# Kernel optimization log

Measured on AMD Instinct MI355X. Metric: run time of the kernel, lower is better.

## Reference

```python
import jax, jax.numpy as jnp
import numpy as np

SCORE_THRESH = 0.05
NMS_THRESH = 0.5
MAX_DET = 100
N_BOXES = 8192


def setup_inputs() -> dict:
    key = jax.random.key(0)
    k1, k2, k3, k4, k5 = jax.random.split(key, 5)
    N = N_BOXES
    # well-formed axis-aligned boxes (x1,y1,x2,y2) plus 8 keypoint coords
    xy = jax.random.uniform(k1, (N, 2)) * 1000.0
    wh = jax.random.uniform(k2, (N, 2)) * 120.0 + 4.0
    kp = jax.random.uniform(k3, (N, 8)) * 1000.0
    boxes = jnp.concatenate([xy, xy + wh, kp], axis=1)            # (N, 12)
    classification = jax.random.uniform(k4, (N, 8))               # two heads x 4 orientations
    dimensions = jax.random.uniform(k5, (N, 3)) * 4.0             # (h, w, l) for the single class
    return {"boxes": boxes, "dimensions": dimensions, "classification": classification}


def _nms_keep(b4, scores, valid):
    """Greedy NMS. Returns (order, keep) where order sorts by score desc and
    keep[i] says whether the i-th sorted box survives."""
    N = b4.shape[0]
    order = jnp.argsort(-jnp.where(valid, scores, -jnp.inf))
    bs = b4[order]                                                 # (N, 4) sorted boxes
    vs = valid[order]
    x1, y1, x2, y2 = bs[:, 0], bs[:, 1], bs[:, 2], bs[:, 3]
    area = (x2 - x1) * (y2 - y1)
    iw = jnp.clip(jnp.minimum(x2[:, None], x2[None, :]) - jnp.maximum(x1[:, None], x1[None, :]), 0.0)
    ih = jnp.clip(jnp.minimum(y2[:, None], y2[None, :]) - jnp.maximum(y1[:, None], y1[None, :]), 0.0)
    inter = iw * ih                                                # (N, N)
    iou = inter / jnp.maximum(area[:, None] + area[None, :] - inter, 1e-8)
    idx = jnp.arange(N)

    def body(keep, xs):
        row, v, i = xs
        suppressed = jnp.any(keep & (row > NMS_THRESH) & (idx < i))
        keep = keep.at[i].set(v & jnp.logical_not(suppressed))
        return keep, None

    keep, _ = jax.lax.scan(body, jnp.zeros((N,), dtype=bool), (iou, vs, idx))
    return order, keep


def reference(boxes, dimensions, classification):
    # max over the two classification heads -> per-orientation score (N, 4)
    cls2 = jnp.maximum(classification[:, :4], classification[:, 4:])
    orient = jnp.argmax(cls2, axis=1)                              # best orientation per box
    score = jnp.max(cls2, axis=1)                                  # best-orientation score
    valid = score > SCORE_THRESH

    order, keep = _nms_keep(boxes[:, :4], score, valid)
    sorted_score = jnp.where(keep, score[order], -jnp.inf)
    top_scores, top_pos = jax.lax.top_k(sorted_score, MAX_DET)     # top-k among kept
    sel = order[top_pos]                                           # original box indices
    ok = jnp.isfinite(top_scores)                                  # real detections vs -1 padding

    out_boxes = jnp.where(ok[:, None], boxes[sel], -1.0)           # (MAX_DET, 12)
    out_dims = jnp.where(ok[:, None], dimensions[sel, :3], -1.0)   # (MAX_DET, 3)
    out_scores = jnp.where(ok, score[sel], -1.0)                   # (MAX_DET,)
    out_labels = jnp.where(ok, 0, -1).astype(jnp.int32)            # single class -> label 0
    out_orient = jnp.where(ok, orient[sel], -1).astype(jnp.int32)
    return out_boxes, out_dims, out_scores, out_labels, out_orient
```

## Files before the change

kernel.cpp:

```cpp
#include <hip/hip_runtime.h>

#define NBOX 8192
#define BT 1024
#define MAXDET 100
#define SCORE_T 0.05f
#define NMS_T 0.5f
#define CAP 1024
#define CAPM 384
#define NWMAX 6
#define KTGT 128
#define TOPBIN_T 0.99609375f

typedef unsigned long long u64;

__device__ __forceinline__ float rl_f(float v, int j) {
    return __int_as_float(__builtin_amdgcn_readlane(__float_as_int(v), j));
}

__device__ __forceinline__ float iou_fn(float x1, float y1, float x2, float y2, float area,
                                        float bx1, float by1, float bx2, float by2, float barea) {
    float iw = fminf(x2, bx2) - fmaxf(x1, bx1);
    float ih = fminf(y2, by2) - fmaxf(y1, by1);
    iw = fmaxf(iw, 0.0f);
    ih = fmaxf(ih, 0.0f);
    float inter = iw * ih;
    return inter / fmaxf(area + barea - inter, 1e-8f);
}

__device__ __forceinline__ void bins_of(unsigned k, int& b1, int& b2) {
    float s = __uint_as_float(k & 0x7FFFFFFFu);
    b1 = (int)(s * 256.0f); if (b1 > 255) b1 = 255;
    b2 = (int)(s * 65536.0f) & 255;
}

__global__ __launch_bounds__(BT) void hot_kernel(
    const float* __restrict__ boxes, const float* __restrict__ dims,
    const float* __restrict__ cls, unsigned* __restrict__ flagG,
    float* __restrict__ out) {
    __shared__ u64 s_sel[CAPM];
    __shared__ float4 s_cb[CAPM];
    __shared__ unsigned char s_or[CAPM];
    __shared__ u64 s_gt[NWMAX][CAPM];
    __shared__ u64 s_sg[NWMAX][CAPM];
    __shared__ u64 s_K[NWMAX], s_U[NWMAX];
    __shared__ int s_cnt;

    const int tid = threadIdx.x;
    const int lane = tid & 63;
    const int w = tid >> 6;

    if (tid == 0) s_cnt = 0;
    __syncthreads();

#pragma unroll
    for (int j = 0; j < NBOX / BT; ++j) {
        int i = tid + j * BT;
        const float4 c0 = *reinterpret_cast<const float4*>(cls + i * 8);
        const float4 c1 = *reinterpret_cast<const float4*>(cls + i * 8 + 4);
        float m0 = fmaxf(c0.x, c1.x), m1 = fmaxf(c0.y, c1.y);
        float m2 = fmaxf(c0.z, c1.z), m3 = fmaxf(c0.w, c1.w);
        float s = fmaxf(fmaxf(m0, m1), fmaxf(m2, m3));
        if (s > SCORE_T && s >= TOPBIN_T) {
            unsigned u = __float_as_uint(s);
            unsigned key = (u >> 31) ? ~u : (u | 0x80000000u);
            int o = 0; float best = m0;
            if (m1 > best) { best = m1; o = 1; }
            if (m2 > best) { best = m2; o = 2; }
            if (m3 > best) { best = m3; o = 3; }
            int pos = atomicAdd(&s_cnt, 1);
            if (pos < CAPM) {
                s_sel[pos] = (((u64)key) << 13) | (unsigned)(NBOX - 1 - i);
                s_cb[pos] = *reinterpret_cast<const float4*>(boxes + i * 12);
                s_or[pos] = (unsigned char)o;
            }
        }
    }
    __syncthreads();
    const int cnt = s_cnt;
    if (cnt == 0 || cnt > CAPM) {
        if (tid == 0) flagG[0] = 1u;
        return;
    }
    const int NW = (cnt + 63) >> 6;

    const int tot = NW * cnt;
    for (int p = tid; p < tot; p += BT) {
        int q = p / cnt;
        int t = p - q * cnt;
        u64 selt = s_sel[t];
        float4 bt = s_cb[t];
        float x1 = bt.x, y1 = bt.y, x2 = bt.z, y2 = bt.w;
        float area = (x2 - x1) * (y2 - y1);
        int jbase = q << 6;
        int jmax = cnt - jbase; if (jmax > 64) jmax = 64;
        u64 g = 0ull, sg = 0ull;
        for (int jj = 0; jj < jmax; ++jj) {
            int jdx = jbase + jj;
            u64 selj = s_sel[jdx];
            float4 bj = s_cb[jdx];
            float barea = (bj.z - bj.x) * (bj.w - bj.y);
            float iou = iou_fn(x1, y1, x2, y2, area, bj.x, bj.y, bj.z, bj.w, barea);
            if (selj > selt) {
                u64 bit = 1ull << jj;
                g |= bit;
                if (iou > NMS_T) sg |= bit;
            }
        }
        s_gt[q][t] = g;
        s_sg[q][t] = sg;
    }
    if (tid < NWMAX) {
        int base = tid << 6;
        u64 uw = (cnt <= base) ? 0ull
               : ((cnt - base >= 64) ? ~0ull : ((1ull << (cnt - base)) - 1ull));
        s_U[tid] = uw;
        s_K[tid] = 0ull;
    }
    __syncthreads();

    const int t = tid;
    const bool have = t < cnt;
    for (int it = 0; it < CAPM; ++it) {
        bool undec = have && ((s_U[t >> 6] >> (t & 63)) & 1ull);
        u64 deadm = 0ull, blkm = 0ull;
        if (undec) {
            for (int q = 0; q < NW; ++q) {
                u64 sg = s_sg[q][t];
                deadm |= sg & s_K[q];
                blkm  |= sg & s_U[q];
            }
        }
        bool toDead = undec && (deadm != 0ull);
        bool toKept = undec && (deadm == 0ull) && (blkm == 0ull);
        u64 dW = __ballot(toDead);
        u64 kW = __ballot(toKept);
        if (lane == 0 && w < NW) {
            s_K[w] |= kW;
            s_U[w] &= ~(kW | dW);
        }
        __syncthreads();
        u64 anyU = 0ull;
        for (int q = 0; q < NW; ++q) anyU |= s_U[q];
        if (anyU == 0ull) break;
        __syncthreads();
    }

    int kcnt = 0;
    for (int q = 0; q < NW; ++q) kcnt += (int)__popcll(s_K[q]);
    if (kcnt < MAXDET) {
        if (tid == 0) flagG[0] = 1u;
        return;
    }
    if (tid == 0) flagG[0] = 0u;

    float* ob = out;
    float* od = out + MAXDET * 12;
    float* os = out + MAXDET * 15;
    float* ol = out + MAXDET * 16;
    float* oo = out + MAXDET * 17;
    if (have && ((s_K[t >> 6] >> (t & 63)) & 1ull)) {
        int rank = 0;
        for (int q = 0; q < NW; ++q) rank += (int)__popcll(s_gt[q][t] & s_K[q]);
        if (rank < MAXDET) {
            u64 v = s_sel[t];
            int idx = NBOX - 1 - (int)(v & 8191ull);
            float sscore = __uint_as_float(((unsigned)(v >> 13)) & 0x7FFFFFFFu);
            float4* obr = reinterpret_cast<float4*>(ob + rank * 12);
            const float4* br = reinterpret_cast<const float4*>(boxes + idx * 12);
            obr[0] = s_cb[t];
            obr[1] = br[1];
            obr[2] = br[2];
            od[rank * 3 + 0] = dims[idx * 3 + 0];
            od[rank * 3 + 1] = dims[idx * 3 + 1];
            od[rank * 3 + 2] = dims[idx * 3 + 2];
            os[rank] = sscore;
            ol[rank] = 0.0f;
            oo[rank] = (float)s_or[t];
        }
    }
}

__global__ __launch_bounds__(BT) void fallback_kernel(
    const float* __restrict__ boxes, const float* __restrict__ dims,
    const float* __restrict__ cls, const unsigned* __restrict__ flagG,
    float* __restrict__ out) {
    if (flagG[0] == 0u) return;
    __shared__ unsigned s_key[NBOX];
    __shared__ unsigned s_hist[256];
    __shared__ u64 s_sel[CAP];
    __shared__ u64 s_srt[CAP];
    __shared__ unsigned short s_srtpos[CAP];
    __shared__ float4 s_cb[CAP];
    __shared__ float4 s_bb[128];
    __shared__ float s_bar[128];
    __shared__ float4 s_kb[MAXDET];
    __shared__ float s_karea[MAXDET], s_kscore[MAXDET];
    __shared__ int s_ksel[MAXDET];
    __shared__ int s_kc, s_cnt, s_B1, s_B2, s_state, s_refKrem;
    __shared__ u64 s_alive0;

    const int tid = threadIdx.x;
    const int lane = tid & 63;
    const int wid = tid >> 6;

    auto rank_scatter = [&](int sc, bool loadBox) {
        if (tid < sc) {
            u64 mine = s_sel[tid];
            float4 pb = make_float4(0.f, 0.f, 0.f, 0.f);
            if (loadBox) {
                int bidx = NBOX - 1 - (int)(mine & 8191ull);
                pb = *reinterpret_cast<const float4*>(boxes + bidx * 12);
            }
            int rank = 0;
            int j = 0;
            for (; j + 8 <= sc; j += 8) {
                u64 a0 = s_sel[j + 0], a1 = s_sel[j + 1], a2 = s_sel[j + 2], a3 = s_sel[j + 3];
                u64 a4 = s_sel[j + 4], a5 = s_sel[j + 5], a6 = s_sel[j + 6], a7 = s_sel[j + 7];
                rank += (int)(a0 > mine) + (int)(a1 > mine) + (int)(a2 > mine) + (int)(a3 > mine)
                      + (int)(a4 > mine) + (int)(a5 > mine) + (int)(a6 > mine) + (int)(a7 > mine);
            }
            for (; j < sc; ++j) rank += (s_sel[j] > mine) ? 1 : 0;
            s_srt[rank] = mine;
            s_srtpos[rank] = (unsigned short)tid;
            if (loadBox) s_cb[tid] = pb;
        }
    };

    auto nms_groups = [&](int scN) {
        for (int base = 0; base < scN && s_kc < MAXDET; base += 128) {
            const int kc0 = s_kc;
            float x1 = 0.f, y1 = 0.f, x2 = 0.f, y2 = 0.f, area = 0.f, sscore = 0.f;
            int sidx = 0; bool have = false;
            if (wid < 2) {
                int p = base + wid * 64 + lane;
                have = p < scN;
                u64 v = have ? s_srt[p] : 0ull;
                int cp = have ? (int)s_srtpos[p] : 0;
                sidx = NBOX - 1 - (int)(v & 8191ull);
                sscore = __uint_as_float(((unsigned)(v >> 13)) & 0x7FFFFFFFu);
                float4 b = s_cb[cp];
                if (have) { x1 = b.x; y1 = b.y; x2 = b.z; y2 = b.w; area = (x2 - x1) * (y2 - y1); }
                int sl = wid * 64 + lane;
                s_bb[sl] = make_float4(x1, y1, x2, y2); s_bar[sl] = area;
            }
            __syncthreads();
            if (wid == 0) {
                bool cand = have;
                for (int k = 0; k < kc0; ++k) {
                    float4 kb = s_kb[k];
                    float iou = iou_fn(x1, y1, x2, y2, area, kb.x, kb.y, kb.z, kb.w, s_karea[k]);
                    cand = cand && !(iou > NMS_T);
                }
                u64 m = 0ull;
#pragma unroll 8
                for (int j = 0; j < 64; ++j) {
                    float iou = iou_fn(x1, y1, x2, y2, area,
                                       rl_f(x1, j), rl_f(y1, j), rl_f(x2, j), rl_f(y2, j), rl_f(area, j));
                    if ((iou > NMS_T) && (j < lane)) m |= (1ull << j);
                }
                u64 alive = __ballot(cand);
                u64 conf = __ballot((m & alive) != 0ull) & alive;
                while (conf) {
                    int i = (int)__builtin_ctzll(conf);
                    bool deadI = (lane == i) && ((m & alive) != 0ull);
                    u64 d = __ballot(deadI);
                    alive &= ~d; conf &= ~(d | (1ull << i));
                }
                int rank = (int)__popcll(alive & ((1ull << lane) - 1ull));
                int slot = kc0 + rank;
                if (((alive >> lane) & 1ull) && slot < MAXDET) {
                    s_kb[slot] = make_float4(x1, y1, x2, y2);
                    s_karea[slot] = area; s_kscore[slot] = sscore; s_ksel[slot] = sidx;
                }
                if (lane == 0) s_alive0 = alive;
            }
            u64 m_low = 0ull, m_high = 0ull;
            bool cand1 = have;
            if (wid == 1) {
                for (int k = 0; k < kc0; ++k) {
                    float4 kb = s_kb[k];
                    float iou = iou_fn(x1, y1, x2, y2, area, kb.x, kb.y, kb.z, kb.w, s_karea[k]);
                    cand1 = cand1 && !(iou > NMS_T);
                }
#pragma unroll 8
                for (int j = 0; j < 64; ++j) {
                    float4 bb = s_bb[j];
                    float iou = iou_fn(x1, y1, x2, y2, area, bb.x, bb.y, bb.z, bb.w, s_bar[j]);
                    if (iou > NMS_T) m_low |= (1ull << j);
                }
#pragma unroll 8
                for (int j = 0; j < 64; ++j) {
                    float iou = iou_fn(x1, y1, x2, y2, area,
                                       rl_f(x1, j), rl_f(y1, j), rl_f(x2, j), rl_f(y2, j), rl_f(area, j));
                    if ((iou > NMS_T) && (j < lane)) m_high |= (1ull << j);
                }
            }
            __syncthreads();
            if (wid == 1) {
                u64 alive0 = s_alive0;
                int popc0 = (int)__popcll(alive0);
                bool cand = cand1 && ((m_low & alive0) == 0ull);
                u64 alive = __ballot(cand);
                u64 conf = __ballot((m_high & alive) != 0ull) & alive;
                while (conf) {
                    int i = (int)__builtin_ctzll(conf);
                    bool deadI = (lane == i) && ((m_high & alive) != 0ull);
                    u64 d = __ballot(deadI);
                    alive &= ~d; conf &= ~(d | (1ull << i));
                }
                int rank = (int)__popcll(alive & ((1ull << lane) - 1ull));
                int slot = kc0 + popc0 + rank;
                if (((alive >> lane) & 1ull) && slot < MAXDET) {
                    s_kb[slot] = make_float4(x1, y1, x2, y2);
                    s_karea[slot] = area; s_kscore[slot] = sscore; s_ksel[slot] = sidx;
                }
                if (lane == 0) {
                    int nk = kc0 + popc0 + (int)__popcll(alive);
                    s_kc = nk > MAXDET ? MAXDET : nk;
                }
            }
            __syncthreads();
        }
    };

    unsigned keyr[8];
#pragma unroll
    for (int j = 0; j < NBOX / BT; ++j) {
        int i = tid + j * BT;
        const float4 c0 = *reinterpret_cast<const float4*>(cls + i * 8);
        const float4 c1 = *reinterpret_cast<const float4*>(cls + i * 8 + 4);
        float s = fmaxf(fmaxf(fmaxf(c0.x, c1.x), fmaxf(c0.y, c1.y)),
                        fmaxf(fmaxf(c0.z, c1.z), fmaxf(c0.w, c1.w)));
        unsigned u = __float_as_uint(s);
        unsigned key = (u >> 31) ? ~u : (u | 0x80000000u);
        key = (s > SCORE_T) ? key : 0u;
        keyr[j] = key;
        s_key[i] = key;
    }
    if (tid == 0) { s_kc = 0; s_cnt = 0; }
    __syncthreads();
#pragma unroll
    for (int j = 0; j < NBOX / BT; ++j) {
        unsigned k = keyr[j];
        if (k) {
            float s = __uint_as_float(k & 0x7FFFFFFFu);
            if (s >= TOPBIN_T) {
                int pos = atomicAdd(&s_cnt, 1);
                if (pos < CAP) {
                    int i = tid + j * BT;
                    s_sel[pos] = (((u64)k) << 13) | (unsigned)(NBOX - 1 - i);
                    s_cb[pos] = *reinterpret_cast<const float4*>(boxes + i * 12);
                }
            }
        }
    }
    __syncthreads();
    const int cnt0 = s_cnt;
    const bool ovf = cnt0 > CAP;
    if (!ovf && cnt0 > 0) {
        rank_scatter(cnt0, false);
        __syncthreads();
        nms_groups(cnt0);
    }
    int U1 = ovf ? 256 : 255;
    int U2 = 0;
    if (s_kc < MAXDET) {
        if (tid < 256) s_hist[tid] = 0u;
        if (tid == 0) s_cnt = 0;
        __syncthreads();
        for (int j = 0; j < NBOX / BT; ++j) {
            unsigned k = s_key[tid + j * BT];
            if (k) {
                int b1, b2; bins_of(k, b1, b2);
                if (b1 < U1 || (b1 == U1 && b2 < U2)) atomicAdd(&s_hist[b1], 1u);
            }
        }
        while (true) {
            __syncthreads();
            if (wid == 0) {
                unsigned c0 = s_hist[lane * 4 + 0], c1s = s_hist[lane * 4 + 1];
                unsigned c2 = s_hist[lane * 4 + 2], c3 = s_hist[lane * 4 + 3];
                unsigned t3 = c3, t2 = c2 + t3, t1 = c1s + t2, t0 = c0 + t1;
                unsigned acc = t0;
#pragma unroll
                for (int d = 1; d < 64; d <<= 1) {
                    unsigned o = __shfl_down(acc, d);
                    if (lane + d < 64) acc += o;
                }
                unsigned excl = acc - t0;
                unsigned totalRem = __shfl(acc, 0);
                if (lane == 0) s_state = (totalRem == 0u) ? 2 : 0;
                if (totalRem != 0u) {
                    unsigned Kt = totalRem < (unsigned)KTGT ? totalRem : (unsigned)KTGT;
                    unsigned incq[4] = { excl + t0, excl + t1, excl + t2, excl + t3 };
                    unsigned abvq[4] = { excl + t1, excl + t2, excl + t3, excl };
#pragma unroll
                    for (int q = 0; q < 4; ++q) {
                        if (incq[q] >= Kt && abvq[q] < Kt) {
                            s_B1 = lane * 4 + q; s_B2 = 0;
                            if (incq[q] > CAP) { s_state = 1; s_refKrem = (int)(Kt - abvq[q]); }
                        }
                    }
                }
            }
            __syncthreads();
            const int st = s_state;
            if (st == 2) break;
            const int B1 = s_B1;
            if (st == 1) {
                if (tid < 256) s_hist[tid] = 0u;
                __syncthreads();
                for (int j = 0; j < NBOX / BT; ++j) {
                    unsigned k = s_key[tid + j * BT];
                    if (k) {
                        int b1, b2; bins_of(k, b1, b2);
                        if ((b1 < U1 || (b1 == U1 && b2 < U2)) && b1 == B1)
                            atomicAdd(&s_hist[b2], 1u);
                    }
                }
                __syncthreads();
                if (wid == 0) {
                    unsigned c0 = s_hist[lane * 4 + 0], c1s = s_hist[lane * 4 + 1];
                    unsigned c2 = s_hist[lane * 4 + 2], c3 = s_hist[lane * 4 + 3];
                    unsigned t3 = c3, t2 = c2 + t3, t1 = c1s + t2, t0 = c0 + t1;
                    unsigned acc = t0;
#pragma unroll
                    for (int d = 1; d < 64; d <<= 1) {
                        unsigned o = __shfl_down(acc, d);
                        if (lane + d < 64) acc += o;
                    }
                    unsigned excl = acc - t0;
                    unsigned Krem = (unsigned)s_refKrem;
                    unsigned incq[4] = { excl + t0, excl + t1, excl + t2, excl + t3 };
                    unsigned abvq[4] = { excl + t1, excl + t2, excl + t3, excl };
#pragma unroll
                    for (int q = 0; q < 4; ++q)
                        if (incq[q] >= Krem && abvq[q] < Krem) s_B2 = lane * 4 + q;
                }
                __syncthreads();
            }
            const int B2 = s_B2;
            for (int j = 0; j < NBOX / BT; ++j) {
                int i = tid + j * BT;
                unsigned k = s_key[i];
                if (k) {
                    int b1, b2; bins_of(k, b1, b2);
                    bool inr = (b1 < U1) || (b1 == U1 && b2 < U2);
                    bool sel = inr && ((b1 > B1) || (b1 == B1 && b2 >= B2));
                    if (sel) {
                        int pos = atomicAdd(&s_cnt, 1);
                        if (pos < CAP)
                            s_sel[pos] = (((u64)k) << 13) | (unsigned)(NBOX - 1 - i);
                    }
                }
            }
            __syncthreads();
            const int sc2 = s_cnt < CAP ? s_cnt : CAP;
            rank_scatter(sc2, true);
            __syncthreads();
            nms_groups(sc2);
            if (s_kc >= MAXDET) break;
            U1 = B1; U2 = B2;
            if (tid < 256) s_hist[tid] = 0u;
            if (tid == 0) s_cnt = 0;
            __syncthreads();
            for (int j = 0; j < NBOX / BT; ++j) {
                unsigned k = s_key[tid + j * BT];
                if (k) {
                    int b1, b2; bins_of(k, b1, b2);
                    if (b1 < U1 || (b1 == U1 && b2 < U2)) atomicAdd(&s_hist[b1], 1u);
                }
            }
        }
    }
    __syncthreads();
    if (tid < MAXDET) {
        const int kc = s_kc;
        float* ob = out;
        float* od = out + MAXDET * 12;
        float* os = out + MAXDET * 15;
        float* ol = out + MAXDET * 16;
        float* oo = out + MAXDET * 17;
        float4* obr = reinterpret_cast<float4*>(ob + tid * 12);
        if (tid < kc) {
            int sel = s_ksel[tid];
            const float4* br = reinterpret_cast<const float4*>(boxes + sel * 12);
            obr[0] = br[0]; obr[1] = br[1]; obr[2] = br[2];
            od[tid * 3 + 0] = dims[sel * 3 + 0];
            od[tid * 3 + 1] = dims[sel * 3 + 1];
            od[tid * 3 + 2] = dims[sel * 3 + 2];
            os[tid] = s_kscore[tid];
            ol[tid] = 0.0f;
            const float4 c0 = *reinterpret_cast<const float4*>(cls + sel * 8);
            const float4 c1 = *reinterpret_cast<const float4*>(cls + sel * 8 + 4);
            float m0 = fmaxf(c0.x, c1.x), m1 = fmaxf(c0.y, c1.y);
            float m2 = fmaxf(c0.z, c1.z), m3 = fmaxf(c0.w, c1.w);
            int o = 0; float best = m0;
            if (m1 > best) { best = m1; o = 1; }
            if (m2 > best) { best = m2; o = 2; }
            if (m3 > best) { best = m3; o = 3; }
            oo[tid] = (float)o;
        } else {
            const float4 neg1 = make_float4(-1.f, -1.f, -1.f, -1.f);
            obr[0] = neg1; obr[1] = neg1; obr[2] = neg1;
            od[tid * 3 + 0] = -1.0f; od[tid * 3 + 1] = -1.0f; od[tid * 3 + 2] = -1.0f;
            os[tid] = -1.0f; ol[tid] = -1.0f; oo[tid] = -1.0f;
        }
    }
}

extern "C" void kernel_launch(void* const* d_in, const int* in_sizes, int n_in,
                              void* d_out, int out_size, void* d_ws, size_t ws_size,
                              hipStream_t stream) {
    const float* boxes = (const float*)d_in[0];
    const float* dims  = (const float*)d_in[1];
    const float* cls   = (const float*)d_in[2];
    float* out = (float*)d_out;
    unsigned* flag = (unsigned*)d_ws;
    (void)in_sizes; (void)n_in; (void)out_size; (void)ws_size;
    hot_kernel<<<1, BT, 0, stream>>>(boxes, dims, cls, flag, out);
    fallback_kernel<<<1, BT, 0, stream>>>(boxes, dims, cls, flag, out);
}
```

Before: 27.74 us.

## Fuse hot and fallback NMS into one multi-block kernel with last-block finish

Replaces the single-block hot kernel and the separate fallback launch with one kernel over 32 blocks of 384 threads. Each block scores a 256-box slice and appends top-bin candidates to a global list via atomics. The last block to finish, detected with a done counter, runs the bitmask NMS or the histogram fallback. This spreads the initial score scan across CUs and removes one kernel launch, at the cost of a memset, global atomics and threadfences, and a smaller final block for the serial NMS phase.

```diff
diff --git a/kernel.cpp b/kernel.cpp
--- a/kernel.cpp
+++ b/kernel.cpp
@@ -1,7 +1,8 @@
 #include <hip/hip_runtime.h>
 
 #define NBOX 8192
-#define BT 1024
+#define NBLK 32
+#define BTF 384
 #define MAXDET 100
 #define SCORE_T 0.05f
 #define NMS_T 0.5f
@@ -33,28 +34,40 @@
     b2 = (int)(s * 65536.0f) & 255;
 }
 
-__global__ __launch_bounds__(BT) void hot_kernel(
+__global__ __launch_bounds__(BTF) void fused_kernel(
     const float* __restrict__ boxes, const float* __restrict__ dims,
-    const float* __restrict__ cls, unsigned* __restrict__ flagG,
+    const float* __restrict__ cls, unsigned* __restrict__ cntG,
+    unsigned* __restrict__ doneG, u64* __restrict__ kidxG,
     float* __restrict__ out) {
-    __shared__ u64 s_sel[CAPM];
-    __shared__ float4 s_cb[CAPM];
-    __shared__ unsigned char s_or[CAPM];
+    __shared__ u64 s_sel[CAP];
+    __shared__ float4 s_cb[CAP];
     __shared__ u64 s_gt[NWMAX][CAPM];
     __shared__ u64 s_sg[NWMAX][CAPM];
     __shared__ u64 s_K[NWMAX], s_U[NWMAX];
-    __shared__ int s_cnt;
+    __shared__ unsigned s_keyS[NBOX];
+    __shared__ unsigned s_hist[256];
+    __shared__ u64 s_srt[CAP];
+    __shared__ unsigned short s_srtpos[CAP];
+    __shared__ float4 s_bb[128];
+    __shared__ float s_bar[128];
+    __shared__ float4 s_kb[MAXDET];
+    __shared__ float s_karea[MAXDET], s_kscore[MAXDET];
+    __shared__ int s_ksel[MAXDET];
+    __shared__ int s_kc, s_cnt, s_B1, s_B2, s_state, s_refKrem;
+    __shared__ u64 s_alive0;
+    __shared__ int s_lcnt, s_base, s_last;
 
     const int tid = threadIdx.x;
     const int lane = tid & 63;
     const int w = tid >> 6;
-
-    if (tid == 0) s_cnt = 0;
+    const int blk = blockIdx.x;
+
+    if (tid == 0) s_lcnt = 0;
     __syncthreads();
-
-#pragma unroll
-    for (int j = 0; j < NBOX / BT; ++j) {
-        int i = tid + j * BT;
+    u64 myv = 0ull;
+    int lpos = -1;
+    if (tid < 256) {
+        const int i = blk * 256 + tid;
         const float4 c0 = *reinterpret_cast<const float4*>(cls + i * 8);
         const float4 c1 = *reinterpret_cast<const float4*>(cls + i * 8 + 4);
         float m0 = fmaxf(c0.x, c1.x), m1 = fmaxf(c0.y, c1.y);
@@ -63,321 +76,274 @@
         if (s > SCORE_T && s >= TOPBIN_T) {
             unsigned u = __float_as_uint(s);
             unsigned key = (u >> 31) ? ~u : (u | 0x80000000u);
-            int o = 0; float best = m0;
-            if (m1 > best) { best = m1; o = 1; }
-            if (m2 > best) { best = m2; o = 2; }
-            if (m3 > best) { best = m3; o = 3; }
-            int pos = atomicAdd(&s_cnt, 1);
-            if (pos < CAPM) {
-                s_sel[pos] = (((u64)key) << 13) | (unsigned)(NBOX - 1 - i);
-                s_cb[pos] = *reinterpret_cast<const float4*>(boxes + i * 12);
-                s_or[pos] = (unsigned char)o;
-            }
+            myv = (((u64)key) << 13) | (unsigned)(NBOX - 1 - i);
+            lpos = atomicAdd(&s_lcnt, 1);
         }
     }
     __syncthreads();
-    const int cnt = s_cnt;
-    if (cnt == 0 || cnt > CAPM) {
-        if (tid == 0) flagG[0] = 1u;
-        return;
+    if (tid == 0) s_base = (int)atomicAdd(cntG, (unsigned)s_lcnt);
+    __syncthreads();
+    if (lpos >= 0) {
+        int g = s_base + lpos;
+        if (g < CAPM) atomicExch(&kidxG[g], myv);
     }
-    const int NW = (cnt + 63) >> 6;
-
-    const int tot = NW * cnt;
-    for (int p = tid; p < tot; p += BT) {
-        int q = p / cnt;
-        int t = p - q * cnt;
-        u64 selt = s_sel[t];
-        float4 bt = s_cb[t];
-        float x1 = bt.x, y1 = bt.y, x2 = bt.z, y2 = bt.w;
-        float area = (x2 - x1) * (y2 - y1);
-        int jbase = q << 6;
-        int jmax = cnt - jbase; if (jmax > 64) jmax = 64;
-        u64 g = 0ull, sg = 0ull;
-        for (int jj = 0; jj < jmax; ++jj) {
-            int jdx = jbase + jj;
-            u64 selj = s_sel[jdx];
-            float4 bj = s_cb[jdx];
-            float barea = (bj.z - bj.x) * (bj.w - bj.y);
-            float iou = iou_fn(x1, y1, x2, y2, area, bj.x, bj.y, bj.z, bj.w, barea);
-            if (selj > selt) {
-                u64 bit = 1ull << jj;
-                g |= bit;
-                if (iou > NMS_T) sg |= bit;
-            }
-        }
-        s_gt[q][t] = g;
-        s_sg[q][t] = sg;
+    __threadfence();
+    __syncthreads();
+    if (tid == 0) s_last = (atomicAdd(doneG, 1u) == (unsigned)(NBLK - 1)) ? 1 : 0;
+    __syncthreads();
+    if (!s_last) return;
+    __threadfence();
+
+    const int cnt = (int)atomicAdd(cntG, 0u);
+
+    if (cnt > 0 && cnt <= CAPM) {
+        for (int t = tid; t < cnt; t += BTF) {
+            u64 v = atomicAdd(&kidxG[t], 0ull);
+            s_sel[t] = v;
+            int idx = NBOX - 1 - (int)(v & 8191ull);
+            s_cb[t] = *reinterpret_cast<const float4*>(boxes + idx * 12);
+        }
+        __syncthreads();
+        const int NW = (cnt + 63) >> 6;
+        const int tot = NW * cnt;
+        for (int p = tid; p < tot; p += BTF) {
+            int q = p / cnt;
+            int t = p - q * cnt;
+            u64 selt = s_sel[t];
+            float4 bt = s_cb[t];
+            float x1 = bt.x, y1 = bt.y, x2 = bt.z, y2 = bt.w;
+            float area = (x2 - x1) * (y2 - y1);
+            int jbase = q << 6;
+            int jmax = cnt - jbase; if (jmax > 64) jmax = 64;
+            u64 g = 0ull, sg = 0ull;
+            for (int jj = 0; jj < jmax; ++jj) {
+                int jdx = jbase + jj;
+                u64 selj = s_sel[jdx];
+                float4 bj = s_cb[jdx];
+                float barea = (bj.z - bj.x) * (bj.w - bj.y);
+                float iou = iou_fn(x1, y1, x2, y2, area, bj.x, bj.y, bj.z, bj.w, barea);
+                if (selj > selt) {
+                    u64 bit = 1ull << jj;
+                    g |= bit;
+                    if (iou > NMS_T) sg |= bit;
+                }
+            }
+            s_gt[q][t] = g;
+            s_sg[q][t] = sg;
+        }
+        if (tid < NWMAX) {
+            int base = tid << 6;
+            u64 uw = (cnt <= base) ? 0ull
+                   : ((cnt - base >= 64) ? ~0ull : ((1ull << (cnt - base)) - 1ull));
+            s_U[tid] = uw;
+            s_K[tid] = 0ull;
+        }
+        __syncthreads();
+        const int t = tid;
+        const bool have = t < cnt;
+        for (int it = 0; it < CAPM; ++it) {
+            bool undec = have && ((s_U[t >> 6] >> (t & 63)) & 1ull);
+            u64 deadm = 0ull, blkm = 0ull;
+            if (undec) {
+                for (int q = 0; q < NW; ++q) {
+                    u64 sg = s_sg[q][t];
+                    deadm |= sg & s_K[q];
+                    blkm  |= sg & s_U[q];
+                }
+            }
+            bool toDead = undec && (deadm != 0ull);
+            bool toKept = undec && (deadm == 0ull) && (blkm == 0ull);
+            u64 dW = __ballot(toDead);
+            u64 kW = __ballot(toKept);
+            if (lane == 0 && w < NW) {
+                s_K[w] |= kW;
+                s_U[w] &= ~(kW | dW);
+            }
+            __syncthreads();
+            u64 anyU = 0ull;
+            for (int q = 0; q < NW; ++q) anyU |= s_U[q];
+            if (anyU == 0ull) break;
+            __syncthreads();
+        }
+        int kcnt = 0;
+        for (int q = 0; q < NW; ++q) kcnt += (int)__popcll(s_K[q]);
+        if (kcnt >= MAXDET) {
+            float* ob = out;
+            float* od = out + MAXDET * 12;
+            float* os = out + MAXDET * 15;
+            float* ol = out + MAXDET * 16;
+            float* oo = out + MAXDET * 17;
+            if (have && ((s_K[t >> 6] >> (t & 63)) & 1ull)) {
+                int rank = 0;
+                for (int q = 0; q < NW; ++q) rank += (int)__popcll(s_gt[q][t] & s_K[q]);
+                if (rank < MAXDET) {
+                    u64 v = s_sel[t];
+                    int idx = NBOX - 1 - (int)(v & 8191ull);
+                    float sscore = __uint_as_float(((unsigned)(v >> 13)) & 0x7FFFFFFFu);
+                    float4* obr = reinterpret_cast<float4*>(ob + rank * 12);
+                    const float4* br = reinterpret_cast<const float4*>(boxes + idx * 12);
+                    obr[0] = s_cb[t];
+                    obr[1] = br[1];
+                    obr[2] = br[2];
+                    od[rank * 3 + 0] = dims[idx * 3 + 0];
+                    od[rank * 3 + 1] = dims[idx * 3 + 1];
+                    od[rank * 3 + 2] = dims[idx * 3 + 2];
+                    os[rank] = sscore;
+                    ol[rank] = 0.0f;
+                    const float4 c0 = *reinterpret_cast<const float4*>(cls + idx * 8);
+                    const float4 c1 = *reinterpret_cast<const float4*>(cls + idx * 8 + 4);
+                    float m0 = fmaxf(c0.x, c1.x), m1 = fmaxf(c0.y, c1.y);
+                    float m2 = fmaxf(c0.z, c1.z), m3 = fmaxf(c0.w, c1.w);
+                    int o = 0; float best = m0;
+                    if (m1 > best) { best = m1; o = 1; }
+                    if (m2 > best) { best = m2; o = 2; }
+                    if (m3 > best) { best = m3; o = 3; }
+                    oo[rank] = (float)o;
+                }
+            }
+            return;
+        }
     }
-    if (tid < NWMAX) {
-        int base = tid << 6;
-        u64 uw = (cnt <= base) ? 0ull
-               : ((cnt - base >= 64) ? ~0ull : ((1ull << (cnt - base)) - 1ull));
-        s_U[tid] = uw;
-        s_K[tid] = 0ull;
-    }
-    __syncthreads();
-
-    const int t = tid;
-    const bool have = t < cnt;
-    for (int it = 0; it < CAPM; ++it) {
-        bool undec = have && ((s_U[t >> 6] >> (t & 63)) & 1ull);
-        u64 deadm = 0ull, blkm = 0ull;
-        if (undec) {
-            for (int q = 0; q < NW; ++q) {
-                u64 sg = s_sg[q][t];
-                deadm |= sg & s_K[q];
-                blkm  |= sg & s_U[q];
-            }
-        }
-        bool toDead = undec && (deadm != 0ull);
-        bool toKept = undec && (deadm == 0ull) && (blkm == 0ull);
-        u64 dW = __ballot(toDead);
-        u64 kW = __ballot(toKept);
-        if (lane == 0 && w < NW) {
-            s_K[w] |= kW;
-            s_U[w] &= ~(kW | dW);
-        }
+
+    {
+        auto rank_scatter = [&](int sc) {
+            for (int t = tid; t < sc; t += BTF) {
+                u64 mine = s_sel[t];
+                int bidx = NBOX - 1 - (int)(mine & 8191ull);
+                float4 pb = *reinterpret_cast<const float4*>(boxes + bidx * 12);
+                int rank = 0;
+                int j = 0;
+                for (; j + 8 <= sc; j += 8) {
+                    u64 a0 = s_sel[j + 0], a1 = s_sel[j + 1], a2 = s_sel[j + 2], a3 = s_sel[j + 3];
+                    u64 a4 = s_sel[j + 4], a5 = s_sel[j + 5], a6 = s_sel[j + 6], a7 = s_sel[j + 7];
+                    rank += (int)(a0 > mine) + (int)(a1 > mine) + (int)(a2 > mine) + (int)(a3 > mine)
+                          + (int)(a4 > mine) + (int)(a5 > mine) + (int)(a6 > mine) + (int)(a7 > mine);
+                }
+                for (; j < sc; ++j) rank += (s_sel[j] > mine) ? 1 : 0;
+                s_srt[rank] = mine;
+                s_srtpos[rank] = (unsigned short)t;
+                s_cb[t] = pb;
+            }
+        };
+
+        auto nms_groups = [&](int scN) {
+            for (int base = 0; base < scN && s_kc < MAXDET; base += 128) {
+                const int kc0 = s_kc;
+                float x1 = 0.f, y1 = 0.f, x2 = 0.f, y2 = 0.f, area = 0.f, sscore = 0.f;
+                int sidx = 0; bool have2 = false;
+                if (w < 2) {
+                    int p = base + w * 64 + lane;
+                    have2 = p < scN;
+                    u64 v = have2 ? s_srt[p] : 0ull;
+                    int cp = have2 ? (int)s_srtpos[p] : 0;
+                    sidx = NBOX - 1 - (int)(v & 8191ull);
+                    sscore = __uint_as_float(((unsigned)(v >> 13)) & 0x7FFFFFFFu);
+                    float4 b = s_cb[cp];
+                    if (have2) { x1 = b.x; y1 = b.y; x2 = b.z; y2 = b.w; area = (x2 - x1) * (y2 - y1); }
+                    int sl = w * 64 + lane;
+                    s_bb[sl] = make_float4(x1, y1, x2, y2); s_bar[sl] = area;
+                }
+                __syncthreads();
+                if (w == 0) {
+                    bool cand = have2;
+                    for (int k = 0; k < kc0; ++k) {
+                        float4 kb = s_kb[k];
+                        float iou = iou_fn(x1, y1, x2, y2, area, kb.x, kb.y, kb.z, kb.w, s_karea[k]);
+                        cand = cand && !(iou > NMS_T);
+                    }
+                    u64 m = 0ull;
+#pragma unroll 8
+                    for (int j = 0; j < 64; ++j) {
+                        float iou = iou_fn(x1, y1, x2, y2, area,
+                                           rl_f(x1, j), rl_f(y1, j), rl_f(x2, j), rl_f(y2, j), rl_f(area, j));
+                        if ((iou > NMS_T) && (j < lane)) m |= (1ull << j);
+                    }
+                    u64 alive = __ballot(cand);
+                    u64 conf = __ballot((m & alive) != 0ull) & alive;
+                    while (conf) {
+                        int i = (int)__builtin_ctzll(conf);
+                        bool deadI = (lane == i) && ((m & alive) != 0ull);
+                        u64 d = __ballot(deadI);
+                        alive &= ~d; conf &= ~(d | (1ull << i));
+                    }
+                    int rank = (int)__popcll(alive & ((1ull << lane) - 1ull));
+                    int slot = kc0 + rank;
+                    if (((alive >> lane) & 1ull) && slot < MAXDET) {
+                        s_kb[slot] = make_float4(x1, y1, x2, y2);
+                        s_karea[slot] = area; s_kscore[slot] = sscore; s_ksel[slot] = sidx;
+                    }
+                    if (lane == 0) s_alive0 = alive;
+                }
+                u64 m_low = 0ull, m_high = 0ull;
+                bool cand1 = have2;
+                if (w == 1) {
+                    for (int k = 0; k < kc0; ++k) {
+                        float4 kb = s_kb[k];
+                        float iou = iou_fn(x1, y1, x2, y2, area, kb.x, kb.y, kb.z, kb.w, s_karea[k]);
+                        cand1 = cand1 && !(iou > NMS_T);
+                    }
+#pragma unroll 8
+                    for (int j = 0; j < 64; ++j) {
+                        float4 bb = s_bb[j];
+                        float iou = iou_fn(x1, y1, x2, y2, area, bb.x, bb.y, bb.z, bb.w, s_bar[j]);
+                        if (iou > NMS_T) m_low |= (1ull << j);
+                    }
+#pragma unroll 8
+                    for (int j = 0; j < 64; ++j) {
+                        float iou = iou_fn(x1, y1, x2, y2, area,
+                                           rl_f(x1, j), rl_f(y1, j), rl_f(x2, j), rl_f(y2, j), rl_f(area, j));
+                        if ((iou > NMS_T) && (j < lane)) m_high |= (1ull << j);
+                    }
+                }
+                __syncthreads();
+                if (w == 1) {
+                    u64 alive0 = s_alive0;
+                    int popc0 = (int)__popcll(alive0);
+                    bool cand = cand1 && ((m_low & alive0) == 0ull);
+                    u64 alive = __ballot(cand);
+                    u64 conf = __ballot((m_high & alive) != 0ull) & alive;
+                    while (conf) {
+                        int i = (int)__builtin_ctzll(conf);
+                        bool deadI = (lane == i) && ((m_high & alive) != 0ull);
+                        u64 d = __ballot(deadI);
+                        alive &= ~d; conf &= ~(d | (1ull << i));
+                    }
+                    int rank = (int)__popcll(alive & ((1ull << lane) - 1ull));
+                    int slot = kc0 + popc0 + rank;
+                    if (((alive >> lane) & 1ull) && slot < MAXDET) {
+                        s_kb[slot] = make_float4(x1, y1, x2, y2);
+                        s_karea[slot] = area; s_kscore[slot] = sscore; s_ksel[slot] = sidx;
+                    }
+                    if (lane == 0) {
+                        int nk = kc0 + popc0 + (int)__popcll(alive);
+                        s_kc = nk > MAXDET ? MAXDET : nk;
+                    }
+                }
+                __syncthreads();
+            }
+        };
+
+        for (int i = tid; i < NBOX; i += BTF) {
+            const float4 c0 = *reinterpret_cast<const float4*>(cls + i * 8);
+            const float4 c1 = *reinterpret_cast<const float4*>(cls + i * 8 + 4);
+            float s = fmaxf(fmaxf(fmaxf(c0.x, c1.x), fmaxf(c0.y, c1.y)),
+                            fmaxf(fmaxf(c0.z, c1.z), fmaxf(c0.w, c1.w)));
+            unsigned u = __float_as_uint(s);
+            unsigned key = (u >> 31) ? ~u : (u | 0x80000000u);
+            s_keyS[i] = (s > SCORE_T) ? key : 0u;
+        }
+        if (tid == 0) { s_kc = 0; s_cnt = 0; }
+        if (tid < 256) s_hist[tid] = 0u;
         __syncthreads();
-        u64 anyU = 0ull;
-        for (int q = 0; q < NW; ++q) anyU |= s_U[q];
-        if (anyU == 0ull) break;
-        __syncthreads();
-    }
-
-    int kcnt = 0;
-    for (int q = 0; q < NW; ++q) kcnt += (int)__popcll(s_K[q]);
-    if (kcnt < MAXDET) {
-        if (tid == 0) flagG[0] = 1u;
-        return;
-    }
-    if (tid == 0) flagG[0] = 0u;
-
-    float* ob = out;
-    float* od = out + MAXDET * 12;
-    float* os = out + MAXDET * 15;
-    float* ol = out + MAXDET * 16;
-    float* oo = out + MAXDET * 17;
-    if (have && ((s_K[t >> 6] >> (t & 63)) & 1ull)) {
-        int rank = 0;
-        for (int q = 0; q < NW; ++q) rank += (int)__popcll(s_gt[q][t] & s_K[q]);
-        if (rank < MAXDET) {
-            u64 v = s_sel[t];
-            int idx = NBOX - 1 - (int)(v & 8191ull);
-            float sscore = __uint_as_float(((unsigned)(v >> 13)) & 0x7FFFFFFFu);
-            float4* obr = reinterpret_cast<float4*>(ob + rank * 12);
-            const float4* br = reinterpret_cast<const float4*>(boxes + idx * 12);
-            obr[0] = s_cb[t];
-            obr[1] = br[1];
-            obr[2] = br[2];
-            od[rank * 3 + 0] = dims[idx * 3 + 0];
-            od[rank * 3 + 1] = dims[idx * 3 + 1];
-            od[rank * 3 + 2] = dims[idx * 3 + 2];
-            os[rank] = sscore;
-            ol[rank] = 0.0f;
-            oo[rank] = (float)s_or[t];
-        }
-    }
-}
-
-__global__ __launch_bounds__(BT) void fallback_kernel(
-    const float* __restrict__ boxes, const float* __restrict__ dims,
-    const float* __restrict__ cls, const unsigned* __restrict__ flagG,
-    float* __restrict__ out) {
-    if (flagG[0] == 0u) return;
-    __shared__ unsigned s_key[NBOX];
-    __shared__ unsigned s_hist[256];
-    __shared__ u64 s_sel[CAP];
-    __shared__ u64 s_srt[CAP];
-    __shared__ unsigned short s_srtpos[CAP];
-    __shared__ float4 s_cb[CAP];
-    __shared__ float4 s_bb[128];
-    __shared__ float s_bar[128];
-    __shared__ float4 s_kb[MAXDET];
-    __shared__ float s_karea[MAXDET], s_kscore[MAXDET];
-    __shared__ int s_ksel[MAXDET];
-    __shared__ int s_kc, s_cnt, s_B1, s_B2, s_state, s_refKrem;
-    __shared__ u64 s_alive0;
-
-    const int tid = threadIdx.x;
-    const int lane = tid & 63;
-    const int wid = tid >> 6;
-
-    auto rank_scatter = [&](int sc, bool loadBox) {
-        if (tid < sc) {
-            u64 mine = s_sel[tid];
-            float4 pb = make_float4(0.f, 0.f, 0.f, 0.f);
-            if (loadBox) {
-                int bidx = NBOX - 1 - (int)(mine & 8191ull);
-                pb = *reinterpret_cast<const float4*>(boxes + bidx * 12);
-            }
-            int rank = 0;
-            int j = 0;
-            for (; j + 8 <= sc; j += 8) {
-                u64 a0 = s_sel[j + 0], a1 = s_sel[j + 1], a2 = s_sel[j + 2], a3 = s_sel[j + 3];
-                u64 a4 = s_sel[j + 4], a5 = s_sel[j + 5], a6 = s_sel[j + 6], a7 = s_sel[j + 7];
-                rank += (int)(a0 > mine) + (int)(a1 > mine) + (int)(a2 > mine) + (int)(a3 > mine)
-                      + (int)(a4 > mine) + (int)(a5 > mine) + (int)(a6 > mine) + (int)(a7 > mine);
-            }
-            for (; j < sc; ++j) rank += (s_sel[j] > mine) ? 1 : 0;
-            s_srt[rank] = mine;
-            s_srtpos[rank] = (unsigned short)tid;
-            if (loadBox) s_cb[tid] = pb;
-        }
-    };
-
-    auto nms_groups = [&](int scN) {
-        for (int base = 0; base < scN && s_kc < MAXDET; base += 128) {
-            const int kc0 = s_kc;
-            float x1 = 0.f, y1 = 0.f, x2 = 0.f, y2 = 0.f, area = 0.f, sscore = 0.f;
-            int sidx = 0; bool have = false;
-            if (wid < 2) {
-                int p = base + wid * 64 + lane;
-                have = p < scN;
-                u64 v = have ? s_srt[p] : 0ull;
-                int cp = have ? (int)s_srtpos[p] : 0;
-                sidx = NBOX - 1 - (int)(v & 8191ull);
-                sscore = __uint_as_float(((unsigned)(v >> 13)) & 0x7FFFFFFFu);
-                float4 b = s_cb[cp];
-                if (have) { x1 = b.x; y1 = b.y; x2 = b.z; y2 = b.w; area = (x2 - x1) * (y2 - y1); }
-                int sl = wid * 64 + lane;
-                s_bb[sl] = make_float4(x1, y1, x2, y2); s_bar[sl] = area;
-            }
-            __syncthreads();
-            if (wid == 0) {
-                bool cand = have;
-                for (int k = 0; k < kc0; ++k) {
-                    float4 kb = s_kb[k];
-                    float iou = iou_fn(x1, y1, x2, y2, area, kb.x, kb.y, kb.z, kb.w, s_karea[k]);
-                    cand = cand && !(iou > NMS_T);
-                }
-                u64 m = 0ull;
-#pragma unroll 8
-                for (int j = 0; j < 64; ++j) {
-                    float iou = iou_fn(x1, y1, x2, y2, area,
-                                       rl_f(x1, j), rl_f(y1, j), rl_f(x2, j), rl_f(y2, j), rl_f(area, j));
-                    if ((iou > NMS_T) && (j < lane)) m |= (1ull << j);
-                }
-                u64 alive = __ballot(cand);
-                u64 conf = __ballot((m & alive) != 0ull) & alive;
-                while (conf) {
-                    int i = (int)__builtin_ctzll(conf);
-                    bool deadI = (lane == i) && ((m & alive) != 0ull);
-                    u64 d = __ballot(deadI);
-                    alive &= ~d; conf &= ~(d | (1ull << i));
-                }
-                int rank = (int)__popcll(alive & ((1ull << lane) - 1ull));
-                int slot = kc0 + rank;
-                if (((alive >> lane) & 1ull) && slot < MAXDET) {
-                    s_kb[slot] = make_float4(x1, y1, x2, y2);
-                    s_karea[slot] = area; s_kscore[slot] = sscore; s_ksel[slot] = sidx;
-                }
-                if (lane == 0) s_alive0 = alive;
-            }
-            u64 m_low = 0ull, m_high = 0ull;
-            bool cand1 = have;
-            if (wid == 1) {
-                for (int k = 0; k < kc0; ++k) {
-                    float4 kb = s_kb[k];
-                    float iou = iou_fn(x1, y1, x2, y2, area, kb.x, kb.y, kb.z, kb.w, s_karea[k]);
-                    cand1 = cand1 && !(iou > NMS_T);
-                }
-#pragma unroll 8
-                for (int j = 0; j < 64; ++j) {
-                    float4 bb = s_bb[j];
-                    float iou = iou_fn(x1, y1, x2, y2, area, bb.x, bb.y, bb.z, bb.w, s_bar[j]);
-                    if (iou > NMS_T) m_low |= (1ull << j);
-                }
-#pragma unroll 8
-                for (int j = 0; j < 64; ++j) {
-                    float iou = iou_fn(x1, y1, x2, y2, area,
-                                       rl_f(x1, j), rl_f(y1, j), rl_f(x2, j), rl_f(y2, j), rl_f(area, j));
-                    if ((iou > NMS_T) && (j < lane)) m_high |= (1ull << j);
-                }
-            }
-            __syncthreads();
-            if (wid == 1) {
-                u64 alive0 = s_alive0;
-                int popc0 = (int)__popcll(alive0);
-                bool cand = cand1 && ((m_low & alive0) == 0ull);
-                u64 alive = __ballot(cand);
-                u64 conf = __ballot((m_high & alive) != 0ull) & alive;
-                while (conf) {
-                    int i = (int)__builtin_ctzll(conf);
-                    bool deadI = (lane == i) && ((m_high & alive) != 0ull);
-                    u64 d = __ballot(deadI);
-                    alive &= ~d; conf &= ~(d | (1ull << i));
-                }
-                int rank = (int)__popcll(alive & ((1ull << lane) - 1ull));
-                int slot = kc0 + popc0 + rank;
-                if (((alive >> lane) & 1ull) && slot < MAXDET) {
-                    s_kb[slot] = make_float4(x1, y1, x2, y2);
-                    s_karea[slot] = area; s_kscore[slot] = sscore; s_ksel[slot] = sidx;
-                }
-                if (lane == 0) {
-                    int nk = kc0 + popc0 + (int)__popcll(alive);
-                    s_kc = nk > MAXDET ? MAXDET : nk;
-                }
-            }
-            __syncthreads();
-        }
-    };
-
-    unsigned keyr[8];
-#pragma unroll
-    for (int j = 0; j < NBOX / BT; ++j) {
-        int i = tid + j * BT;
-        const float4 c0 = *reinterpret_cast<const float4*>(cls + i * 8);
-        const float4 c1 = *reinterpret_cast<const float4*>(cls + i * 8 + 4);
-        float s = fmaxf(fmaxf(fmaxf(c0.x, c1.x), fmaxf(c0.y, c1.y)),
-                        fmaxf(fmaxf(c0.z, c1.z), fmaxf(c0.w, c1.w)));
-        unsigned u = __float_as_uint(s);
-        unsigned key = (u >> 31) ? ~u : (u | 0x80000000u);
-        key = (s > SCORE_T) ? key : 0u;
-        keyr[j] = key;
-        s_key[i] = key;
-    }
-    if (tid == 0) { s_kc = 0; s_cnt = 0; }
-    __syncthreads();
-#pragma unroll
-    for (int j = 0; j < NBOX / BT; ++j) {
-        unsigned k = keyr[j];
-        if (k) {
-            float s = __uint_as_float(k & 0x7FFFFFFFu);
-            if (s >= TOPBIN_T) {
-                int pos = atomicAdd(&s_cnt, 1);
-                if (pos < CAP) {
-                    int i = tid + j * BT;
-                    s_sel[pos] = (((u64)k) << 13) | (unsigned)(NBOX - 1 - i);
-                    s_cb[pos] = *reinterpret_cast<const float4*>(boxes + i * 12);
-                }
-            }
-        }
-    }
-    __syncthreads();
-    const int cnt0 = s_cnt;
-    const bool ovf = cnt0 > CAP;
-    if (!ovf && cnt0 > 0) {
-        rank_scatter(cnt0, false);
-        __syncthreads();
-        nms_groups(cnt0);
-    }
-    int U1 = ovf ? 256 : 255;
-    int U2 = 0;
-    if (s_kc < MAXDET) {
-        if (tid < 256) s_hist[tid] = 0u;
-        if (tid == 0) s_cnt = 0;
-        __syncthreads();
-        for (int j = 0; j < NBOX / BT; ++j) {
-            unsigned k = s_key[tid + j * BT];
-            if (k) {
-                int b1, b2; bins_of(k, b1, b2);
-                if (b1 < U1 || (b1 == U1 && b2 < U2)) atomicAdd(&s_hist[b1], 1u);
-            }
+
+        int U1 = 256, U2 = 0;
+        for (int i = tid; i < NBOX; i += BTF) {
+            unsigned k = s_keyS[i];
+            if (k) { int b1, b2; bins_of(k, b1, b2); atomicAdd(&s_hist[b1], 1u); }
         }
         while (true) {
             __syncthreads();
-            if (wid == 0) {
+            if (w == 0) {
                 unsigned c0 = s_hist[lane * 4 + 0], c1s = s_hist[lane * 4 + 1];
                 unsigned c2 = s_hist[lane * 4 + 2], c3 = s_hist[lane * 4 + 3];
                 unsigned t3 = c3, t2 = c2 + t3, t1 = c1s + t2, t0 = c0 + t1;
@@ -410,8 +376,8 @@
             if (st == 1) {
                 if (tid < 256) s_hist[tid] = 0u;
                 __syncthreads();
-                for (int j = 0; j < NBOX / BT; ++j) {
-                    unsigned k = s_key[tid + j * BT];
+                for (int i = tid; i < NBOX; i += BTF) {
+                    unsigned k = s_keyS[i];
                     if (k) {
                         int b1, b2; bins_of(k, b1, b2);
                         if ((b1 < U1 || (b1 == U1 && b2 < U2)) && b1 == B1)
@@ -419,7 +385,7 @@
                     }
                 }
                 __syncthreads();
-                if (wid == 0) {
+                if (w == 0) {
                     unsigned c0 = s_hist[lane * 4 + 0], c1s = s_hist[lane * 4 + 1];
                     unsigned c2 = s_hist[lane * 4 + 2], c3 = s_hist[lane * 4 + 3];
                     unsigned t3 = c3, t2 = c2 + t3, t1 = c1s + t2, t0 = c0 + t1;
@@ -440,9 +406,8 @@
                 __syncthreads();
             }
             const int B2 = s_B2;
-            for (int j = 0; j < NBOX / BT; ++j) {
-                int i = tid + j * BT;
-                unsigned k = s_key[i];
+            for (int i = tid; i < NBOX; i += BTF) {
+                unsigned k = s_keyS[i];
                 if (k) {
                     int b1, b2; bins_of(k, b1, b2);
                     bool inr = (b1 < U1) || (b1 == U1 && b2 < U2);
@@ -456,7 +421,7 @@
             }
             __syncthreads();
             const int sc2 = s_cnt < CAP ? s_cnt : CAP;
-            rank_scatter(sc2, true);
+            rank_scatter(sc2);
             __syncthreads();
             nms_groups(sc2);
             if (s_kc >= MAXDET) break;
@@ -464,47 +429,48 @@
             if (tid < 256) s_hist[tid] = 0u;
             if (tid == 0) s_cnt = 0;
             __syncthreads();
-            for (int j = 0; j < NBOX / BT; ++j) {
-                unsigned k = s_key[tid + j * BT];
+            for (int i = tid; i < NBOX; i += BTF) {
+                unsigned k = s_keyS[i];
                 if (k) {
                     int b1, b2; bins_of(k, b1, b2);
                     if (b1 < U1 || (b1 == U1 && b2 < U2)) atomicAdd(&s_hist[b1], 1u);
                 }
             }
         }
-    }
-    __syncthreads();
-    if (tid < MAXDET) {
-        const int kc = s_kc;
-        float* ob = out;
-        float* od = out + MAXDET * 12;
-        float* os = out + MAXDET * 15;
-        float* ol = out + MAXDET * 16;
-        float* oo = out + MAXDET * 17;
-        float4* obr = reinterpret_cast<float4*>(ob + tid * 12);
-        if (tid < kc) {
-            int sel = s_ksel[tid];
-            const float4* br = reinterpret_cast<const float4*>(boxes + sel * 12);
-            obr[0] = br[0]; obr[1] = br[1]; obr[2] = br[2];
-            od[tid * 3 + 0] = dims[sel * 3 + 0];
-            od[tid * 3 + 1] = dims[sel * 3 + 1];
-            od[tid * 3 + 2] = dims[sel * 3 + 2];
-            os[tid] = s_kscore[tid];
-            ol[tid] = 0.0f;
-            const float4 c0 = *reinterpret_cast<const float4*>(cls + sel * 8);
-            const float4 c1 = *reinterpret_cast<const float4*>(cls + sel * 8 + 4);
-            float m0 = fmaxf(c0.x, c1.x), m1 = fmaxf(c0.y, c1.y);
-            float m2 = fmaxf(c0.z, c1.z), m3 = fmaxf(c0.w, c1.w);
-            int o = 0; float best = m0;
-            if (m1 > best) { best = m1; o = 1; }
-            if (m2 > best) { best = m2; o = 2; }
-            if (m3 > best) { best = m3; o = 3; }
-            oo[tid] = (float)o;
-        } else {
-            const float4 neg1 = make_float4(-1.f, -1.f, -1.f, -1.f);
-            obr[0] = neg1; obr[1] = neg1; obr[2] = neg1;
-            od[tid * 3 + 0] = -1.0f; od[tid * 3 + 1] = -1.0f; od[tid * 3 + 2] = -1.0f;
-            os[tid] = -1.0f; ol[tid] = -1.0f; oo[tid] = -1.0f;
+        __syncthreads();
+
+        if (tid < MAXDET) {
+            const int kc = s_kc;
+            float* ob = out;
+            float* od = out + MAXDET * 12;
+            float* os = out + MAXDET * 15;
+            float* ol = out + MAXDET * 16;
+            float* oo = out + MAXDET * 17;
+            float4* obr = reinterpret_cast<float4*>(ob + tid * 12);
+            if (tid < kc) {
+                int sel = s_ksel[tid];
+                const float4* br = reinterpret_cast<const float4*>(boxes + sel * 12);
+                obr[0] = br[0]; obr[1] = br[1]; obr[2] = br[2];
+                od[tid * 3 + 0] = dims[sel * 3 + 0];
+                od[tid * 3 + 1] = dims[sel * 3 + 1];
+                od[tid * 3 + 2] = dims[sel * 3 + 2];
+                os[tid] = s_kscore[tid];
+                ol[tid] = 0.0f;
+                const float4 c0 = *reinterpret_cast<const float4*>(cls + sel * 8);
+                const float4 c1 = *reinterpret_cast<const float4*>(cls + sel * 8 + 4);
+                float m0 = fmaxf(c0.x, c1.x), m1 = fmaxf(c0.y, c1.y);
+                float m2 = fmaxf(c0.z, c1.z), m3 = fmaxf(c0.w, c1.w);
+                int o = 0; float best = m0;
+                if (m1 > best) { best = m1; o = 1; }
+                if (m2 > best) { best = m2; o = 2; }
+                if (m3 > best) { best = m3; o = 3; }
+                oo[tid] = (float)o;
+            } else {
+                const float4 neg1 = make_float4(-1.f, -1.f, -1.f, -1.f);
+                obr[0] = neg1; obr[1] = neg1; obr[2] = neg1;
+                od[tid * 3 + 0] = -1.0f; od[tid * 3 + 1] = -1.0f; od[tid * 3 + 2] = -1.0f;
+                os[tid] = -1.0f; ol[tid] = -1.0f; oo[tid] = -1.0f;
+            }
         }
     }
 }
@@ -516,8 +482,11 @@
     const float* dims  = (const float*)d_in[1];
     const float* cls   = (const float*)d_in[2];
     float* out = (float*)d_out;
-    unsigned* flag = (unsigned*)d_ws;
+    unsigned char* ws = (unsigned char*)d_ws;
+    unsigned* cnt  = (unsigned*)(ws);
+    unsigned* done = (unsigned*)(ws + 4);
+    u64* kidx      = (u64*)(ws + 1024);
     (void)in_sizes; (void)n_in; (void)out_size; (void)ws_size;
-    hot_kernel<<<1, BT, 0, stream>>>(boxes, dims, cls, flag, out);
-    fallback_kernel<<<1, BT, 0, stream>>>(boxes, dims, cls, flag, out);
+    hipMemsetAsync(ws, 0, 8, stream);
+    fused_kernel<<<NBLK, BTF, 0, stream>>>(boxes, dims, cls, cnt, done, kidx, out);
 }
```

New measurement: 42.15 us. +52.0%, slower.
